# Kernel optimization log

Hardware: AMD Instinct MI355X
Metric: run time of the kernel (lower is better)

Reference implementation:

```python
import jax, jax.numpy as jnp
import numpy as np

B, T, D, H, C = 8, 512, 1024, 16, 10   # batch, seq (T_out+1), d=nb_lon*nb_lat, heads, classes
L = 4                                   # effective layers = n - 1 (ModuleLists hold n-1 entries)
DH = D // H
RD = float(np.sqrt(D))
EPS = 1e-5


def make_pos():
    # pos[t, 2k] = sin((t+1)*w_k), pos[t, 2k+1] = sin((t+1)*w_k + pi/2)
    t = np.arange(1, T + 1, dtype=np.float32)[:, None]          # [T,1]
    kk = np.arange(D // 2, dtype=np.float32)
    omega = np.repeat(1.0 / 1000.0 ** (2.0 * kk / D), 2)[None]  # [1,D]
    phase = np.tile(np.array([0.0, np.pi / 2], dtype=np.float32), D // 2)[None]
    return jnp.asarray(np.sin(t * omega + phase), dtype=jnp.float32)


def setup_inputs() -> dict:
    key = jax.random.key(0)
    ks = jax.random.split(key, 12)
    s = 0.02
    inp = {
        'x': jax.random.normal(ks[0], (B, T, D), jnp.float32),
        'k': jax.random.normal(ks[1], (B, H, T, DH), jnp.float32),
        'v': jax.random.normal(ks[2], (B, H, T, DH), jnp.float32),
        'pos': make_pos(),
        'Wq1': jax.random.normal(ks[3], (L, D, D), jnp.float32) * s,
        'Wk1': jax.random.normal(ks[4], (L, D, D), jnp.float32) * s,
        'Wv1': jax.random.normal(ks[5], (L, D, D), jnp.float32) * s,
        'Wq2': jax.random.normal(ks[6], (L, D, D), jnp.float32) * s,
        'Wfc': jax.random.normal(ks[7], (L, D, D), jnp.float32) * s,
        'bfc': jnp.zeros((L, D), jnp.float32),
        'g1': jnp.ones((L - 1, D), jnp.float32),
        'b1': jnp.zeros((L - 1, D), jnp.float32),
        'g2': jnp.ones((L, D), jnp.float32),
        'b2': jnp.zeros((L, D), jnp.float32),
        'g3': jnp.ones((L, D), jnp.float32),
        'b3': jnp.zeros((L, D), jnp.float32),
        # xavier_uniform on [1, C-1]
        'cutoff': jax.random.uniform(ks[8], (1, C - 1), jnp.float32,
                                     -np.sqrt(6.0 / C), np.sqrt(6.0 / C)),
    }
    return inp


def _ln(x, g, b):
    m = jnp.mean(x, axis=-1, keepdims=True)
    var = jnp.var(x, axis=-1, keepdims=True)
    return (x - m) / jnp.sqrt(var + EPS) * g + b


def _self_attn(x, Wq, Wk, Wv):
    # nn.Linear: y = x @ W.T ; no causal mask (masking defaults to False)
    q = (x @ Wq.T).reshape(B, T, H, DH)
    kk = (x @ Wk.T).reshape(B, T, H, DH)
    vv = (x @ Wv.T).reshape(B, T, H, DH)
    a = jnp.einsum('bqhe,bkhe->bhqk', q, kk) / RD
    a = jax.nn.softmax(a, axis=-1)
    o = jnp.einsum('bhqk,bkhe->bqhe', a, vv).reshape(B, T, D)
    return x + o


def _cross_attn(x, Wq, k, v, mask):
    q = (x @ Wq.T).reshape(B, T, H, DH)
    a = jnp.einsum('bqhe,bhke->bhqk', q, k) / RD
    a = jnp.where(mask, -jnp.inf, a)  # causal mask on cross scores (intended semantics)
    a = jax.nn.softmax(a, axis=-1)
    o = jnp.einsum('bhqk,bhke->bqhe', a, v).reshape(B, T, D)
    return x + o


def reference(x, k, v, pos, Wq1, Wk1, Wv1, Wq2, Wfc, bfc,
              g1, b1, g2, b2, g3, b3, cutoff):
    x = x + pos
    mask = jnp.triu(jnp.ones((T, T), bool), 1)
    for i in range(L):
        if i != 0:
            x = _ln(x, g1[i - 1], b1[i - 1])
        x = _self_attn(x, Wq1[i], Wk1[i], Wv1[i])
        x = _ln(x, g2[i], b2[i])
        x = _cross_attn(x, Wq2[i], k, v, mask)
        x = _ln(x, g3[i], b3[i])
        x = jax.nn.relu(x @ Wfc[i].T + bfc[i]) + x
    # ordinal sigmoid head: cumulative cutoffs, adjacent sigmoid differences
    b = jnp.cumsum(jnp.concatenate([cutoff[:, :1], cutoff[:, 1:] ** 2], axis=1), axis=1)  # [1,C-1]
    sig = jax.nn.sigmoid(b[0] - x[..., None])  # [B,T,D,C-1]
    probs = jnp.concatenate(
        [sig[..., :1], sig[..., 1:] - sig[..., :-1], 1.0 - sig[..., -1:]], axis=-1)
    return probs
```

## Files before the change

### kernel.cpp

```cpp
#include <hip/hip_runtime.h>


#define BB   8
#define TT   512
#define DD   1024
#define HH   16
#define DHH  64
#define LLAY 4
#define MM   (BB*TT)
#define MD   ((size_t)MM*DD)
#define INV_RD (1.0f/32.0f)
#define LNEPS 1e-5f

typedef unsigned short ushort_t;
typedef __attribute__((ext_vector_type(8))) short short8;
typedef __attribute__((ext_vector_type(4))) float floatx4;

__device__ inline ushort_t f2bf(float f) {
  unsigned u = __builtin_bit_cast(unsigned, f);
  unsigned r = (u + 0x7FFFu + ((u >> 16) & 1u)) >> 16;
  return (ushort_t)r;
}

__global__ __launch_bounds__(256) void cast_all_k(
    const float* __restrict__ Wq1, const float* __restrict__ Wk1,
    const float* __restrict__ Wv1, const float* __restrict__ Wq2f,
    const float* __restrict__ Wfcf, const float* __restrict__ kin,
    const float* __restrict__ vin, const float* __restrict__ x,
    const float* __restrict__ pos,
    ushort_t* __restrict__ wqkv, ushort_t* __restrict__ wq2,
    ushort_t* __restrict__ wfc, ushort_t* __restrict__ kinbf,
    ushort_t* __restrict__ vinbf, float* __restrict__ cur,
    ushort_t* __restrict__ act_bf) {
  int seg = blockIdx.x >> 12;
  size_t j = ((size_t)(blockIdx.x & 4095)) * 256 + threadIdx.x;
  if (seg == 7) {
    int dq  = (int)(j & 255);
    int row = (int)(j >> 8);
    int t   = row & (TT - 1);
    float4 a = ((const float4*)x)[j];
    float4 p = ((const float4*)pos)[(size_t)t * 256 + dq];
    a.x += p.x; a.y += p.y; a.z += p.z; a.w += p.w;
    ((float4*)cur)[j] = a;
    ushort4 b; b.x = f2bf(a.x); b.y = f2bf(a.y); b.z = f2bf(a.z); b.w = f2bf(a.w);
    ((ushort4*)act_bf)[j] = b;
    return;
  }
  const float* src;
  switch (seg) {
    case 0: src = Wq1; break;
    case 1: src = Wk1; break;
    case 2: src = Wv1; break;
    case 3: src = Wq2f; break;
    case 4: src = Wfcf; break;
    case 5: src = kin; break;
    default: src = vin; break;
  }
  float4 v = ((const float4*)src)[j];
  ushort4 o; o.x = f2bf(v.x); o.y = f2bf(v.y); o.z = f2bf(v.z); o.w = f2bf(v.w);
  if (seg < 3) {
    int d4 = (int)(j & 255);
    int n  = (int)((j >> 8) & 1023);
    int i  = (int)(j >> 18);
    size_t drow = (size_t)i * 3072 + (size_t)seg * 1024 + n;
    ((ushort4*)wqkv)[drow * 256 + d4] = o;
  } else {
    ushort_t* dst = (seg == 3) ? wq2 : (seg == 4) ? wfc : (seg == 5) ? kinbf : vinbf;
    ((ushort4*)dst)[j] = o;
  }
}

__global__ __launch_bounds__(256) void ln_k(const float* __restrict__ in,
                                            float* __restrict__ out,
                                            ushort_t* __restrict__ out_bf,
                                            const float* __restrict__ g,
                                            const float* __restrict__ bt) {
  int row = blockIdx.x;
  int t = threadIdx.x;
  const float4* r4 = (const float4*)(in + (size_t)row * DD);
  float4 v = r4[t];
  float s  = v.x + v.y + v.z + v.w;
  float ss = v.x*v.x + v.y*v.y + v.z*v.z + v.w*v.w;
#pragma unroll
  for (int off = 32; off > 0; off >>= 1) {
    s  += __shfl_down(s, off);
    ss += __shfl_down(ss, off);
  }
  __shared__ float red[8];
  int w = t >> 6;
  if ((t & 63) == 0) { red[w] = s; red[4 + w] = ss; }
  __syncthreads();
  s  = red[0] + red[1] + red[2] + red[3];
  ss = red[4] + red[5] + red[6] + red[7];
  float mean = s * (1.0f / DD);
  float var  = ss * (1.0f / DD) - mean * mean;
  float inv  = rsqrtf(var + LNEPS);
  float4 gv = ((const float4*)g)[t];
  float4 bv = ((const float4*)bt)[t];
  float4 o;
  o.x = (v.x - mean) * inv * gv.x + bv.x;
  o.y = (v.y - mean) * inv * gv.y + bv.y;
  o.z = (v.z - mean) * inv * gv.z + bv.z;
  o.w = (v.w - mean) * inv * gv.w + bv.w;
  ((float4*)(out + (size_t)row * DD))[t] = o;
  ushort4 ob; ob.x = f2bf(o.x); ob.y = f2bf(o.y); ob.z = f2bf(o.z); ob.w = f2bf(o.w);
  ((ushort4*)(out_bf + (size_t)row * DD))[t] = ob;
}

__global__ __launch_bounds__(256) void gemm_mfma_bt_k(const ushort_t* __restrict__ A,
                                                      const ushort_t* __restrict__ W,
                                                      ushort_t* __restrict__ Cout,
                                                      int nbx) {
  __shared__ ushort_t As[128 * 32];
  __shared__ ushort_t Bs[128 * 32];
  int t = threadIdx.x;
  int d = blockIdx.x;
  int chunk = gridDim.x >> 3;
  int logical = (d & 7) * chunk + (d >> 3);
  int bx = logical % nbx, by = logical / nbx;
  int n0 = bx * 128, m0 = by * 128;
  int lane = t & 63, w = t >> 6;
  int wm = (w >> 1) * 64, wn = (w & 1) * 64;
  int fr = lane & 15, q = lane >> 4;
  const short8* ap[4]; const short8* bp[4];
#pragma unroll
  for (int i = 0; i < 4; i++) {
    int r  = wm + i * 16 + fr;
    int rn = wn + i * 16 + fr;
    ap[i] = (const short8*)(As + r  * 32 + ((q ^ ((r  >> 1) & 3)) * 8));
    bp[i] = (const short8*)(Bs + rn * 32 + ((q ^ ((rn >> 1) & 3)) * 8));
  }
  auto* As3 = (__attribute__((address_space(3))) ushort_t*)As;
  auto* Bs3 = (__attribute__((address_space(3))) ushort_t*)Bs;
  floatx4 acc[4][4] = {};
  for (int k0 = 0; k0 < DD; k0 += 32) {
    __syncthreads();
#pragma unroll
    for (int j = 0; j < 2; j++) {
      int e = t + j * 256;
      int row = e >> 2, slot = e & 3;
      int c = slot ^ ((row >> 1) & 3);
      const ushort_t* asrc = A + (size_t)(m0 + row) * DD + k0 + c * 8;
      const ushort_t* wsrc = W + (size_t)(n0 + row) * DD + k0 + c * 8;
      __builtin_amdgcn_global_load_lds(
          (const __attribute__((address_space(1))) unsigned*)asrc,
          (__attribute__((address_space(3))) unsigned*)(As3 + e * 8), 16, 0, 0);
      __builtin_amdgcn_global_load_lds(
          (const __attribute__((address_space(1))) unsigned*)wsrc,
          (__attribute__((address_space(3))) unsigned*)(Bs3 + e * 8), 16, 0, 0);
    }
    __syncthreads();
    short8 af[4], bf[4];
#pragma unroll
    for (int i = 0; i < 4; i++) { af[i] = *ap[i]; bf[i] = *bp[i]; }
#pragma unroll
    for (int i = 0; i < 4; i++)
#pragma unroll
      for (int j = 0; j < 4; j++)
        acc[i][j] = __builtin_amdgcn_mfma_f32_16x16x32_bf16(af[i], bf[j], acc[i][j], 0, 0, 0);
  }
  int orow = m0 + wm + q * 4;
  int ocol = n0 + wn + fr;
  int seg = n0 >> 10;
  ushort_t* Cb = Cout + (size_t)seg * MD;
#pragma unroll
  for (int i = 0; i < 4; i++)
#pragma unroll
    for (int j = 0; j < 4; j++)
#pragma unroll
      for (int rr = 0; rr < 4; rr++)
        Cb[(size_t)(orow + i * 16 + rr) * DD + ((ocol + j * 16) & 1023)] =
            f2bf(acc[i][j][rr]);
}

__global__ __launch_bounds__(256) void gemm64_k(const ushort_t* __restrict__ A,
                                                const ushort_t* __restrict__ W,
                                                void* __restrict__ Cout,
                                                const float* __restrict__ bias,
                                                const float* __restrict__ lnres,
                                                const float* __restrict__ cutv,
                                                int mode) {
  __shared__ ushort_t As[128 * 32];
  __shared__ ushort_t Bs[64 * 32];
  int t = threadIdx.x;
  int d = blockIdx.x;
  int logical = (d & 7) * 64 + (d >> 3);
  int bx = logical & 15, by = logical >> 4;
  int n0 = bx * 64, m0 = by * 128;
  int lane = t & 63, w = t >> 6;
  int wm = (w >> 1) * 64, wn = (w & 1) * 32;
  int fr = lane & 15, q = lane >> 4;
  const short8* ap[4]; const short8* bp[2];
#pragma unroll
  for (int i = 0; i < 4; i++) {
    int r = wm + i * 16 + fr;
    ap[i] = (const short8*)(As + r * 32 + ((q ^ ((r >> 1) & 3)) * 8));
  }
#pragma unroll
  for (int j = 0; j < 2; j++) {
    int rn = wn + j * 16 + fr;
    bp[j] = (const short8*)(Bs + rn * 32 + ((q ^ ((rn >> 1) & 3)) * 8));
  }
  auto* As3 = (__attribute__((address_space(3))) ushort_t*)As;
  auto* Bs3 = (__attribute__((address_space(3))) ushort_t*)Bs;
  floatx4 acc[4][2] = {};
  for (int k0 = 0; k0 < DD; k0 += 32) {
    __syncthreads();
#pragma unroll
    for (int j = 0; j < 2; j++) {
      int e = t + j * 256;
      int row = e >> 2, slot = e & 3;
      int c = slot ^ ((row >> 1) & 3);
      const ushort_t* asrc = A + (size_t)(m0 + row) * DD + k0 + c * 8;
      __builtin_amdgcn_global_load_lds(
          (const __attribute__((address_space(1))) unsigned*)asrc,
          (__attribute__((address_space(3))) unsigned*)(As3 + e * 8), 16, 0, 0);
    }
    {
      int e = t;
      int row = e >> 2, slot = e & 3;
      int c = slot ^ ((row >> 1) & 3);
      const ushort_t* wsrc = W + (size_t)(n0 + row) * DD + k0 + c * 8;
      __builtin_amdgcn_global_load_lds(
          (const __attribute__((address_space(1))) unsigned*)wsrc,
          (__attribute__((address_space(3))) unsigned*)(Bs3 + e * 8), 16, 0, 0);
    }
    __syncthreads();
    short8 af[4], bf[2];
#pragma unroll
    for (int i = 0; i < 4; i++) af[i] = *ap[i];
#pragma unroll
    for (int j = 0; j < 2; j++) bf[j] = *bp[j];
#pragma unroll
    for (int i = 0; i < 4; i++)
#pragma unroll
      for (int j = 0; j < 2; j++)
        acc[i][j] = __builtin_amdgcn_mfma_f32_16x16x32_bf16(af[i], bf[j], acc[i][j], 0, 0, 0);
  }
  int orow = m0 + wm + q * 4;
  if (mode == 1) {
    ushort_t* Cb = (ushort_t*)Cout;
#pragma unroll
    for (int i = 0; i < 4; i++)
#pragma unroll
      for (int j = 0; j < 2; j++) {
        int colg = n0 + wn + j * 16 + fr;
#pragma unroll
        for (int rr = 0; rr < 4; rr++)
          Cb[(size_t)(orow + i * 16 + rr) * DD + colg] = f2bf(acc[i][j][rr]);
      }
  } else if (mode == 2) {
    float* C = (float*)Cout;
#pragma unroll
    for (int j = 0; j < 2; j++) {
      int colg = n0 + wn + j * 16 + fr;
      float bv = bias[colg];
#pragma unroll
      for (int i = 0; i < 4; i++)
#pragma unroll
        for (int rr = 0; rr < 4; rr++) {
          size_t idx = (size_t)(orow + i * 16 + rr) * DD + colg;
          C[idx] = fmaxf(acc[i][j][rr] + bv, 0.f) + lnres[idx];
        }
    }
  } else {
    float* H = (float*)Cout;
    float bcum[9];
    bcum[0] = cutv[0];
#pragma unroll
    for (int j = 1; j < 9; j++) { float c = cutv[j]; bcum[j] = bcum[j - 1] + c * c; }
#pragma unroll
    for (int j = 0; j < 2; j++) {
      int colg = n0 + wn + j * 16 + fr;
      float bv = bias[colg];
#pragma unroll
      for (int i = 0; i < 4; i++)
#pragma unroll
        for (int rr = 0; rr < 4; rr++) {
          size_t idx = (size_t)(orow + i * 16 + rr) * DD + colg;
          float xv = fmaxf(acc[i][j][rr] + bv, 0.f) + lnres[idx];
          float ov[10];
          float sp = 1.0f / (1.0f + __expf(xv - bcum[0]));
          ov[0] = sp;
#pragma unroll
          for (int c = 1; c < 9; c++) {
            float sc = 1.0f / (1.0f + __expf(xv - bcum[c]));
            ov[c] = sc - sp;
            sp = sc;
          }
          ov[9] = 1.0f - sp;
          float2* op = (float2*)(H + idx * 10);
#pragma unroll
          for (int c = 0; c < 5; c++) { float2 p; p.x = ov[2 * c]; p.y = ov[2 * c + 1]; op[c] = p; }
        }
    }
  }
}

__global__ __launch_bounds__(256) void attn_mfma_k(const ushort_t* __restrict__ Qb,
                                                   const ushort_t* __restrict__ Kb,
                                                   const ushort_t* __restrict__ Vb,
                                                   const float* __restrict__ resid,
                                                   float* __restrict__ out,
                                                   int cross) {
  __shared__ ushort_t Ks[128 * 64];
  __shared__ ushort_t Vts[64 * 128];
  __shared__ ushort_t QP[64 * 64];
  int t = threadIdx.x, lane = t & 63, w = t >> 6;
  int fr = lane & 15, q8 = lane >> 4;
  int dsp = blockIdx.x;
  int logical = (dsp & 7) * 128 + (dsp >> 3);
  int qt = logical & 7, bh = logical >> 3;
  int b = bh >> 4, h = bh & 15;
  size_t qbase = ((size_t)(b * TT + qt * 64)) * DD + h * DHH;
  size_t kvbase; int kvstride;
  if (cross) { kvbase = (size_t)bh * TT * DHH;          kvstride = DHH; }
  else       { kvbase = (size_t)b * TT * DD + h * DHH;  kvstride = DD;  }

  auto* QP3 = (__attribute__((address_space(3))) ushort_t*)QP;
  auto* Ks3 = (__attribute__((address_space(3))) ushort_t*)Ks;

#pragma unroll
  for (int j = 0; j < 2; j++) {
    int e = t + j * 256;
    int row = e >> 3, slot = e & 7;
    int c = slot ^ (row & 7);
    const ushort_t* src = Qb + qbase + (size_t)row * DD + c * 8;
    __builtin_amdgcn_global_load_lds(
        (const __attribute__((address_space(1))) unsigned*)src,
        (__attribute__((address_space(3))) unsigned*)(QP3 + e * 8), 16, 0, 0);
  }
  __syncthreads();

  short8 qf[2];
#pragma unroll
  for (int ks = 0; ks < 2; ks++) {
    int row = w * 16 + fr;
    int slot = (ks * 4 + q8) ^ (row & 7);
    qf[ks] = *(const short8*)(QP + row * 64 + slot * 8);
  }

  float m_i[4], l_i[4];
  floatx4 o_acc[4] = {};
#pragma unroll
  for (int r = 0; r < 4; r++) { m_i[r] = -1e30f; l_i[r] = 0.f; }

  int nch = cross ? ((qt * 64 + 64 + 127) >> 7) : (TT / 128);
  for (int ch = 0; ch < nch; ch++) {
    __syncthreads();
#pragma unroll
    for (int j = 0; j < 4; j++) {
      int e = t + j * 256;
      int row = e >> 3, slot = e & 7;
      int c = slot ^ (row & 7);
      const ushort_t* src = Kb + kvbase + (size_t)(ch * 128 + row) * kvstride + c * 8;
      __builtin_amdgcn_global_load_lds(
          (const __attribute__((address_space(1))) unsigned*)src,
          (__attribute__((address_space(3))) unsigned*)(Ks3 + e * 8), 16, 0, 0);
    }
    {
      int kp = t & 31, dhg = (t >> 5) * 8;
      const ushort_t* v0 = Vb + kvbase + (size_t)(ch * 128 + 4 * kp) * kvstride + dhg;
      short8 a0 = *(const short8*)v0;
      short8 a1 = *(const short8*)(v0 + kvstride);
      short8 a2 = *(const short8*)(v0 + 2 * kvstride);
      short8 a3 = *(const short8*)(v0 + 3 * kvstride);
#pragma unroll
      for (int j = 0; j < 8; j++) {
        int dh = dhg + j;
        int slot = (kp >> 1) ^ (dh & 15);
        unsigned p01 = (unsigned)(unsigned short)a0[j] |
                       ((unsigned)(unsigned short)a1[j] << 16);
        unsigned p23 = (unsigned)(unsigned short)a2[j] |
                       ((unsigned)(unsigned short)a3[j] << 16);
        uint2 pk; pk.x = p01; pk.y = p23;
        *(uint2*)(Vts + dh * 128 + slot * 8 + (kp & 1) * 4) = pk;
      }
    }
    __syncthreads();

    floatx4 s[8] = {};
    __builtin_amdgcn_s_setprio(1);
#pragma unroll
    for (int nt = 0; nt < 8; nt++) {
      int key = nt * 16 + fr;
#pragma unroll
      for (int ks = 0; ks < 2; ks++) {
        int slot = (ks * 4 + q8) ^ (key & 7);
        short8 kf = *(const short8*)(Ks + key * 64 + slot * 8);
        s[nt] = __builtin_amdgcn_mfma_f32_16x16x32_bf16(qf[ks], kf, s[nt], 0, 0, 0);
      }
    }
    __builtin_amdgcn_s_setprio(0);
    float sv[8][4];
#pragma unroll
    for (int nt = 0; nt < 8; nt++)
#pragma unroll
      for (int r = 0; r < 4; r++)
        sv[nt][r] = s[nt][r] * INV_RD;
    if (cross && ch == nch - 1) {
#pragma unroll
      for (int nt = 0; nt < 8; nt++) {
        int key_g = ch * 128 + nt * 16 + fr;
#pragma unroll
        for (int r = 0; r < 4; r++) {
          int q_g = qt * 64 + w * 16 + q8 * 4 + r;
          if (key_g > q_g) sv[nt][r] = -1e30f;
        }
      }
    }

#pragma unroll
    for (int r = 0; r < 4; r++) {
      float mch = fmaxf(fmaxf(fmaxf(sv[0][r], sv[1][r]), fmaxf(sv[2][r], sv[3][r])),
                        fmaxf(fmaxf(sv[4][r], sv[5][r]), fmaxf(sv[6][r], sv[7][r])));
#pragma unroll
      for (int off = 1; off < 16; off <<= 1) mch = fmaxf(mch, __shfl_xor(mch, off));
      float mn = fmaxf(m_i[r], mch);
      float alpha = __expf(m_i[r] - mn);
      m_i[r] = mn;
      float rs = 0.f;
#pragma unroll
      for (int nt = 0; nt < 8; nt++) {
        float pe = __expf(sv[nt][r] - mn);
        sv[nt][r] = pe; rs += pe;
      }
#pragma unroll
      for (int off = 1; off < 16; off <<= 1) rs += __shfl_xor(rs, off);
      l_i[r] = l_i[r] * alpha + rs;
#pragma unroll
      for (int nt = 0; nt < 4; nt++) o_acc[nt][r] *= alpha;
    }

    ushort_t* Pw = QP + w * 1024;
#pragma unroll
    for (int hf = 0; hf < 2; hf++) {
#pragma unroll
      for (int n4 = 0; n4 < 4; n4++) {
        int col = n4 * 16 + fr;
#pragma unroll
        for (int r = 0; r < 4; r++) {
          int row = q8 * 4 + r;
          int slot = (col >> 3) ^ (row & 7);
          Pw[row * 64 + slot * 8 + (col & 7)] = f2bf(sv[hf * 4 + n4][r]);
        }
      }
      short8 pf[2];
#pragma unroll
      for (int ks = 0; ks < 2; ks++) {
        int slot = (ks * 4 + q8) ^ (fr & 7);
        pf[ks] = *(const short8*)(Pw + fr * 64 + slot * 8);
      }
      __builtin_amdgcn_s_setprio(1);
#pragma unroll
      for (int dnt = 0; dnt < 4; dnt++) {
        int dh = dnt * 16 + fr;
#pragma unroll
        for (int ks = 0; ks < 2; ks++) {
          int vslot = (hf * 8 + ks * 4 + q8) ^ (dh & 15);
          short8 vf = *(const short8*)(Vts + dh * 128 + vslot * 8);
          o_acc[dnt] = __builtin_amdgcn_mfma_f32_16x16x32_bf16(pf[ks], vf, o_acc[dnt], 0, 0, 0);
        }
      }
      __builtin_amdgcn_s_setprio(0);
    }
  }

  float invl[4];
#pragma unroll
  for (int r = 0; r < 4; r++) invl[r] = 1.0f / l_i[r];
#pragma unroll
  for (int nt = 0; nt < 4; nt++) {
#pragma unroll
    for (int r = 0; r < 4; r++) {
      size_t row_g = (size_t)(b * TT + qt * 64 + w * 16 + q8 * 4 + r);
      size_t idx = row_g * DD + h * DHH + nt * 16 + fr;
      out[idx] = resid[idx] + o_acc[nt][r] * invl[r];
    }
  }
}

extern "C" void kernel_launch(void* const* d_in, const int* in_sizes, int n_in,
                              void* d_out, int out_size, void* d_ws, size_t ws_size,
                              hipStream_t stream) {
  (void)in_sizes; (void)n_in; (void)out_size; (void)ws_size;
  const float* x    = (const float*)d_in[0];
  const float* kin  = (const float*)d_in[1];
  const float* vin  = (const float*)d_in[2];
  const float* pos  = (const float*)d_in[3];
  const float* Wq1  = (const float*)d_in[4];
  const float* Wk1  = (const float*)d_in[5];
  const float* Wv1  = (const float*)d_in[6];
  const float* Wq2  = (const float*)d_in[7];
  const float* Wfc  = (const float*)d_in[8];
  const float* bfc  = (const float*)d_in[9];
  const float* g1   = (const float*)d_in[10];
  const float* b1   = (const float*)d_in[11];
  const float* g2   = (const float*)d_in[12];
  const float* b2   = (const float*)d_in[13];
  const float* g3   = (const float*)d_in[14];
  const float* b3   = (const float*)d_in[15];
  const float* cut  = (const float*)d_in[16];
  float* out = (float*)d_out;

  float* cur = (float*)d_ws;
  float* tmp = cur + MD;
  ushort_t* act_bf = (ushort_t*)(tmp + MD);
  ushort_t* qbf    = act_bf + MD;
  ushort_t* kbf    = qbf + MD;
  ushort_t* vbf    = kbf + MD;
  ushort_t* kinbf  = vbf + MD;
  ushort_t* vinbf  = kinbf + MD;
  ushort_t* wqkv   = vinbf + MD;
  ushort_t* wq2    = wqkv + (size_t)LLAY * 3 * DD * DD;
  ushort_t* wfc    = wq2  + (size_t)LLAY * DD * DD;

  dim3 b256(256);

  cast_all_k<<<8 * 4096, b256, 0, stream>>>(Wq1, Wk1, Wv1, Wq2, Wfc, kin, vin,
                                            x, pos, wqkv, wq2, wfc, kinbf, vinbf,
                                            cur, act_bf);

  for (int i = 0; i < LLAY; i++) {
    const float* attn_in;
    if (i) {
      ln_k<<<MM, b256, 0, stream>>>(cur, tmp, act_bf,
                                    g1 + (size_t)(i - 1) * DD, b1 + (size_t)(i - 1) * DD);
      attn_in = tmp;
    } else {
      attn_in = cur;
    }
    gemm_mfma_bt_k<<<768, b256, 0, stream>>>(act_bf, wqkv + (size_t)i * 3 * DD * DD,
                                             qbf, 24);
    attn_mfma_k<<<1024, b256, 0, stream>>>(qbf, kbf, vbf, attn_in, cur, 0);

    ln_k<<<MM, b256, 0, stream>>>(cur, tmp, act_bf,
                                  g2 + (size_t)i * DD, b2 + (size_t)i * DD);
    gemm64_k<<<512, b256, 0, stream>>>(act_bf, wq2 + (size_t)i * DD * DD,
                                       qbf, nullptr, nullptr, nullptr, 1);
    attn_mfma_k<<<1024, b256, 0, stream>>>(qbf, kinbf, vinbf, tmp, cur, 1);

    ln_k<<<MM, b256, 0, stream>>>(cur, tmp, act_bf,
                                  g3 + (size_t)i * DD, b3 + (size_t)i * DD);
    if (i < LLAY - 1) {
      gemm64_k<<<512, b256, 0, stream>>>(act_bf, wfc + (size_t)i * DD * DD,
                                         cur, bfc + (size_t)i * DD, tmp, nullptr, 2);
    } else {
      gemm64_k<<<512, b256, 0, stream>>>(act_bf, wfc + (size_t)i * DD * DD,
                                         out, bfc + (size_t)i * DD, tmp, cut, 3);
    }
  }
}
```

Measured before the change: 979.6 us.

## Store Q/K/V projections head-major and double GEMM K-tile to 64

```diff
diff --git a/kernel.cpp b/kernel.cpp
--- a/kernel.cpp
+++ b/kernel.cpp
@@ -20,6 +20,10 @@
   unsigned u = __builtin_bit_cast(unsigned, f);
   unsigned r = (u + 0x7FFFu + ((u >> 16) & 1u)) >> 16;
   return (ushort_t)r;
+}
+
+__device__ inline size_t bhtd(int m, int cg) {
+  return ((size_t)((m >> 9) * HH + (cg >> 6)) * TT + (m & (TT - 1))) * DHH + (cg & 63);
 }
 
 __global__ __launch_bounds__(256) void cast_all_k(
@@ -111,8 +115,8 @@
                                                       const ushort_t* __restrict__ W,
                                                       ushort_t* __restrict__ Cout,
                                                       int nbx) {
-  __shared__ ushort_t As[128 * 32];
-  __shared__ ushort_t Bs[128 * 32];
+  __shared__ ushort_t As[128 * 64];
+  __shared__ ushort_t Bs[128 * 64];
   int t = threadIdx.x;
   int d = blockIdx.x;
   int chunk = gridDim.x >> 3;
@@ -122,24 +126,19 @@
   int lane = t & 63, w = t >> 6;
   int wm = (w >> 1) * 64, wn = (w & 1) * 64;
   int fr = lane & 15, q = lane >> 4;
-  const short8* ap[4]; const short8* bp[4];
-#pragma unroll
-  for (int i = 0; i < 4; i++) {
-    int r  = wm + i * 16 + fr;
-    int rn = wn + i * 16 + fr;
-    ap[i] = (const short8*)(As + r  * 32 + ((q ^ ((r  >> 1) & 3)) * 8));
-    bp[i] = (const short8*)(Bs + rn * 32 + ((q ^ ((rn >> 1) & 3)) * 8));
-  }
+  int arow[4], brow[4];
+#pragma unroll
+  for (int i = 0; i < 4; i++) { arow[i] = wm + i * 16 + fr; brow[i] = wn + i * 16 + fr; }
   auto* As3 = (__attribute__((address_space(3))) ushort_t*)As;
   auto* Bs3 = (__attribute__((address_space(3))) ushort_t*)Bs;
   floatx4 acc[4][4] = {};
-  for (int k0 = 0; k0 < DD; k0 += 32) {
+  for (int k0 = 0; k0 < DD; k0 += 64) {
     __syncthreads();
 #pragma unroll
-    for (int j = 0; j < 2; j++) {
+    for (int j = 0; j < 4; j++) {
       int e = t + j * 256;
-      int row = e >> 2, slot = e & 3;
-      int c = slot ^ ((row >> 1) & 3);
+      int row = e >> 3, slot = e & 7;
+      int c = slot ^ (row & 7);
       const ushort_t* asrc = A + (size_t)(m0 + row) * DD + k0 + c * 8;
       const ushort_t* wsrc = W + (size_t)(n0 + row) * DD + k0 + c * 8;
       __builtin_amdgcn_global_load_lds(
@@ -150,14 +149,21 @@
           (__attribute__((address_space(3))) unsigned*)(Bs3 + e * 8), 16, 0, 0);
     }
     __syncthreads();
-    short8 af[4], bf[4];
-#pragma unroll
-    for (int i = 0; i < 4; i++) { af[i] = *ap[i]; bf[i] = *bp[i]; }
-#pragma unroll
-    for (int i = 0; i < 4; i++)
-#pragma unroll
-      for (int j = 0; j < 4; j++)
-        acc[i][j] = __builtin_amdgcn_mfma_f32_16x16x32_bf16(af[i], bf[j], acc[i][j], 0, 0, 0);
+#pragma unroll
+    for (int kk = 0; kk < 2; kk++) {
+      short8 af[4], bf[4];
+#pragma unroll
+      for (int i = 0; i < 4; i++) {
+        int ra = arow[i], rb = brow[i];
+        af[i] = *(const short8*)(As + ra * 64 + (((kk * 4 + q) ^ (ra & 7)) * 8));
+        bf[i] = *(const short8*)(Bs + rb * 64 + (((kk * 4 + q) ^ (rb & 7)) * 8));
+      }
+#pragma unroll
+      for (int i = 0; i < 4; i++)
+#pragma unroll
+        for (int j = 0; j < 4; j++)
+          acc[i][j] = __builtin_amdgcn_mfma_f32_16x16x32_bf16(af[i], bf[j], acc[i][j], 0, 0, 0);
+    }
   }
   int orow = m0 + wm + q * 4;
   int ocol = n0 + wn + fr;
@@ -166,11 +172,12 @@
 #pragma unroll
   for (int i = 0; i < 4; i++)
 #pragma unroll
-    for (int j = 0; j < 4; j++)
+    for (int j = 0; j < 4; j++) {
+      int cg = (ocol + j * 16) & 1023;
 #pragma unroll
       for (int rr = 0; rr < 4; rr++)
-        Cb[(size_t)(orow + i * 16 + rr) * DD + ((ocol + j * 16) & 1023)] =
-            f2bf(acc[i][j][rr]);
+        Cb[bhtd(orow + i * 16 + rr, cg)] = f2bf(acc[i][j][rr]);
+    }
 }
 
 __global__ __launch_bounds__(256) void gemm64_k(const ushort_t* __restrict__ A,
@@ -180,8 +187,8 @@
                                                 const float* __restrict__ lnres,
                                                 const float* __restrict__ cutv,
                                                 int mode) {
-  __shared__ ushort_t As[128 * 32];
-  __shared__ ushort_t Bs[64 * 32];
+  __shared__ ushort_t As[128 * 64];
+  __shared__ ushort_t Bs[64 * 64];
   int t = threadIdx.x;
   int d = blockIdx.x;
   int logical = (d & 7) * 64 + (d >> 3);
@@ -190,52 +197,56 @@
   int lane = t & 63, w = t >> 6;
   int wm = (w >> 1) * 64, wn = (w & 1) * 32;
   int fr = lane & 15, q = lane >> 4;
-  const short8* ap[4]; const short8* bp[2];
-#pragma unroll
-  for (int i = 0; i < 4; i++) {
-    int r = wm + i * 16 + fr;
-    ap[i] = (const short8*)(As + r * 32 + ((q ^ ((r >> 1) & 3)) * 8));
-  }
-#pragma unroll
-  for (int j = 0; j < 2; j++) {
-    int rn = wn + j * 16 + fr;
-    bp[j] = (const short8*)(Bs + rn * 32 + ((q ^ ((rn >> 1) & 3)) * 8));
-  }
+  int arow[4], brow[2];
+#pragma unroll
+  for (int i = 0; i < 4; i++) arow[i] = wm + i * 16 + fr;
+#pragma unroll
+  for (int j = 0; j < 2; j++) brow[j] = wn + j * 16 + fr;
   auto* As3 = (__attribute__((address_space(3))) ushort_t*)As;
   auto* Bs3 = (__attribute__((address_space(3))) ushort_t*)Bs;
   floatx4 acc[4][2] = {};
-  for (int k0 = 0; k0 < DD; k0 += 32) {
+  for (int k0 = 0; k0 < DD; k0 += 64) {
     __syncthreads();
 #pragma unroll
-    for (int j = 0; j < 2; j++) {
+    for (int j = 0; j < 4; j++) {
       int e = t + j * 256;
-      int row = e >> 2, slot = e & 3;
-      int c = slot ^ ((row >> 1) & 3);
+      int row = e >> 3, slot = e & 7;
+      int c = slot ^ (row & 7);
       const ushort_t* asrc = A + (size_t)(m0 + row) * DD + k0 + c * 8;
       __builtin_amdgcn_global_load_lds(
           (const __attribute__((address_space(1))) unsigned*)asrc,
           (__attribute__((address_space(3))) unsigned*)(As3 + e * 8), 16, 0, 0);
     }
-    {
-      int e = t;
-      int row = e >> 2, slot = e & 3;
-      int c = slot ^ ((row >> 1) & 3);
+#pragma unroll
+    for (int j = 0; j < 2; j++) {
+      int e = t + j * 256;
+      int row = e >> 3, slot = e & 7;
+      int c = slot ^ (row & 7);
       const ushort_t* wsrc = W + (size_t)(n0 + row) * DD + k0 + c * 8;
       __builtin_amdgcn_global_load_lds(
           (const __attribute__((address_space(1))) unsigned*)wsrc,
           (__attribute__((address_space(3))) unsigned*)(Bs3 + e * 8), 16, 0, 0);
     }
     __syncthreads();
-    short8 af[4], bf[2];
-#pragma unroll
-    for (int i = 0; i < 4; i++) af[i] = *ap[i];
-#pragma unroll
-    for (int j = 0; j < 2; j++) bf[j] = *bp[j];
-#pragma unroll
-    for (int i = 0; i < 4; i++)
-#pragma unroll
-      for (int j = 0; j < 2; j++)
-        acc[i][j] = __builtin_amdgcn_mfma_f32_16x16x32_bf16(af[i], bf[j], acc[i][j], 0, 0, 0);
+#pragma unroll
+    for (int kk = 0; kk < 2; kk++) {
+      short8 af[4], bf[2];
+#pragma unroll
+      for (int i = 0; i < 4; i++) {
+        int ra = arow[i];
+        af[i] = *(const short8*)(As + ra * 64 + (((kk * 4 + q) ^ (ra & 7)) * 8));
+      }
+#pragma unroll
+      for (int j = 0; j < 2; j++) {
+        int rb = brow[j];
+        bf[j] = *(const short8*)(Bs + rb * 64 + (((kk * 4 + q) ^ (rb & 7)) * 8));
+      }
+#pragma unroll
+      for (int i = 0; i < 4; i++)
+#pragma unroll
+        for (int j = 0; j < 2; j++)
+          acc[i][j] = __builtin_amdgcn_mfma_f32_16x16x32_bf16(af[i], bf[j], acc[i][j], 0, 0, 0);
+    }
   }
   int orow = m0 + wm + q * 4;
   if (mode == 1) {
@@ -247,7 +258,7 @@
         int colg = n0 + wn + j * 16 + fr;
 #pragma unroll
         for (int rr = 0; rr < 4; rr++)
-          Cb[(size_t)(orow + i * 16 + rr) * DD + colg] = f2bf(acc[i][j][rr]);
+          Cb[bhtd(orow + i * 16 + rr, colg)] = f2bf(acc[i][j][rr]);
       }
   } else if (mode == 2) {
     float* C = (float*)Cout;
@@ -312,10 +323,8 @@
   int logical = (dsp & 7) * 128 + (dsp >> 3);
   int qt = logical & 7, bh = logical >> 3;
   int b = bh >> 4, h = bh & 15;
-  size_t qbase = ((size_t)(b * TT + qt * 64)) * DD + h * DHH;
-  size_t kvbase; int kvstride;
-  if (cross) { kvbase = (size_t)bh * TT * DHH;          kvstride = DHH; }
-  else       { kvbase = (size_t)b * TT * DD + h * DHH;  kvstride = DD;  }
+  size_t kvbase = (size_t)bh * TT * DHH;
+  size_t qbase  = kvbase + (size_t)qt * 64 * DHH;
 
   auto* QP3 = (__attribute__((address_space(3))) ushort_t*)QP;
   auto* Ks3 = (__attribute__((address_space(3))) ushort_t*)Ks;
@@ -325,7 +334,7 @@
     int e = t + j * 256;
     int row = e >> 3, slot = e & 7;
     int c = slot ^ (row & 7);
-    const ushort_t* src = Qb + qbase + (size_t)row * DD + c * 8;
+    const ushort_t* src = Qb + qbase + (size_t)row * 64 + c * 8;
     __builtin_amdgcn_global_load_lds(
         (const __attribute__((address_space(1))) unsigned*)src,
         (__attribute__((address_space(3))) unsigned*)(QP3 + e * 8), 16, 0, 0);
@@ -353,18 +362,18 @@
       int e = t + j * 256;
       int row = e >> 3, slot = e & 7;
       int c = slot ^ (row & 7);
-      const ushort_t* src = Kb + kvbase + (size_t)(ch * 128 + row) * kvstride + c * 8;
+      const ushort_t* src = Kb + kvbase + (size_t)(ch * 128 + row) * 64 + c * 8;
       __builtin_amdgcn_global_load_lds(
           (const __attribute__((address_space(1))) unsigned*)src,
           (__attribute__((address_space(3))) unsigned*)(Ks3 + e * 8), 16, 0, 0);
     }
     {
       int kp = t & 31, dhg = (t >> 5) * 8;
-      const ushort_t* v0 = Vb + kvbase + (size_t)(ch * 128 + 4 * kp) * kvstride + dhg;
+      const ushort_t* v0 = Vb + kvbase + (size_t)(ch * 128 + 4 * kp) * 64 + dhg;
       short8 a0 = *(const short8*)v0;
-      short8 a1 = *(const short8*)(v0 + kvstride);
-      short8 a2 = *(const short8*)(v0 + 2 * kvstride);
-      short8 a3 = *(const short8*)(v0 + 3 * kvstride);
+      short8 a1 = *(const short8*)(v0 + 64);
+      short8 a2 = *(const short8*)(v0 + 128);
+      short8 a3 = *(const short8*)(v0 + 192);
 #pragma unroll
       for (int j = 0; j < 8; j++) {
         int dh = dhg + j;
```

New measurement: 942.8 us. 1.04x faster.
